# Kernel tuning notes

Hardware: AMD Instinct MI355X
Metric: run time of the kernel (lower is better)

Reference implementation:

```python
import jax, jax.numpy as jnp
import numpy as np
from functools import partial

N, C, D, H, W = 2, 64, 8, 96, 96
G, K, PAD = 2, 3, 1
P = K ** 3
CG = C // G
AXIS_SCALE = jnp.array([0.5, 1.0, 1.0], dtype=jnp.float32)  # applied to (dx, dy, dz)
OFFSET_SCALE = 1.0  # converged warmup scale
EPS = 1e-5


def setup_inputs() -> dict:
    key = jax.random.key(0)
    ks = jax.random.split(key, 13)
    s = 0.05
    return {
        "x": jax.random.normal(ks[0], (N, C, D, H, W), jnp.float32),
        "w_pre": jax.random.normal(ks[1], (C, C), jnp.float32) * s,
        "w_in": jax.random.normal(ks[2], (C, C), jnp.float32) * s,
        "b_in": jnp.zeros((C,), jnp.float32),
        "w_dw": jax.random.normal(ks[3], (C, 1, K, K, K), jnp.float32) * s,
        "w_off": jax.random.normal(ks[4], (C, G * P * 3), jnp.float32) * s,
        "b_off": jnp.zeros((G * P * 3,), jnp.float32),
        "w_mask": jax.random.normal(ks[5], (C, G * P), jnp.float32) * s,
        "b_mask": jnp.zeros((G * P,), jnp.float32),
        "w_out": jax.random.normal(ks[6], (C, C), jnp.float32) * s,
        "b_out": jnp.zeros((C,), jnp.float32),
        "w_post": jax.random.normal(ks[7], (C, C), jnp.float32) * s,
        "gate": jnp.zeros((), jnp.float32),
    }


def _instance_norm(x):  # x: [N, C, D, H, W], normalize over spatial dims per (n, c)
    mean = jnp.mean(x, axis=(2, 3, 4), keepdims=True)
    var = jnp.var(x, axis=(2, 3, 4), keepdims=True)
    return (x - mean) * jax.lax.rsqrt(var + EPS)


def _dcn_core(x_proj, offset, mask):
    # x_proj: [N, D, H, W, C]; offset: [N, D, H, W, G, P, 3] (dx, dy, dz); mask: [N, D, H, W, G, P]
    Dp, Hp, Wp = D + 2 * PAD, H + 2 * PAD, W + 2 * PAD
    x_pad = jnp.pad(x_proj, ((0, 0), (PAD, PAD), (PAD, PAD), (PAD, PAD), (0, 0)))
    x_pad = x_pad.reshape(N, Dp, Hp, Wp, G, CG)

    n_idx = jnp.arange(N).reshape(N, 1, 1, 1, 1)
    g_idx = jnp.arange(G).reshape(1, 1, 1, 1, G)
    zg = jnp.arange(D, dtype=jnp.float32).reshape(1, D, 1, 1, 1)
    yg = jnp.arange(H, dtype=jnp.float32).reshape(1, 1, H, 1, 1)
    xg = jnp.arange(W, dtype=jnp.float32).reshape(1, 1, 1, W, 1)

    def trilinear(zs, ys, xs):  # each [N, D, H, W, G] float coords in padded frame
        z0 = jnp.floor(zs); y0 = jnp.floor(ys); x0 = jnp.floor(xs)
        fz = zs - z0; fy = ys - y0; fx = xs - x0
        z0i = z0.astype(jnp.int32); y0i = y0.astype(jnp.int32); x0i = x0.astype(jnp.int32)
        res = None
        for dz in (0, 1):
            wz = fz if dz else 1.0 - fz
            zi = z0i + dz
            for dy in (0, 1):
                wy = fy if dy else 1.0 - fy
                yi = y0i + dy
                for dx in (0, 1):
                    wx = fx if dx else 1.0 - fx
                    xi = x0i + dx
                    valid = ((zi >= 0) & (zi < Dp) & (yi >= 0) & (yi < Hp)
                             & (xi >= 0) & (xi < Wp)).astype(zs.dtype)
                    g = x_pad[n_idx, jnp.clip(zi, 0, Dp - 1), jnp.clip(yi, 0, Hp - 1),
                              jnp.clip(xi, 0, Wp - 1), g_idx]  # [N,D,H,W,G,CG]
                    term = g * (wz * wy * wx * valid)[..., None]
                    res = term if res is None else res + term
        return res

    # kernel grid points (z-major), base position in padded frame is out_idx + k_idx
    kk = jnp.arange(K, dtype=jnp.float32)
    kz, ky, kx = jnp.meshgrid(kk, kk, kk, indexing="ij")
    kpts = jnp.stack([kz.ravel(), ky.ravel(), kx.ravel()], axis=-1)  # [P, 3]

    off = offset * (AXIS_SCALE * OFFSET_SCALE)  # scale (dx, dy, dz)
    off_p = jnp.moveaxis(off, 5, 0)    # [P, N, D, H, W, G, 3]
    mask_p = jnp.moveaxis(mask, 5, 0)  # [P, N, D, H, W, G]

    def body(acc, inp):
        o, m, kp = inp
        zs = zg + kp[0] + o[..., 2]
        ys = yg + kp[1] + o[..., 1]
        xs = xg + kp[2] + o[..., 0]
        samp = trilinear(zs, ys, xs)  # [N,D,H,W,G,CG]
        return acc + m[..., None] * samp, None

    acc0 = jnp.zeros((N, D, H, W, G, CG), x_proj.dtype)
    acc, _ = jax.lax.scan(body, acc0, (off_p, mask_p, kpts))
    return acc.reshape(N, D, H, W, C)


def _forward(x, w_pre, w_in, b_in, w_dw, w_off, b_off, w_mask, b_mask, w_out, b_out, w_post, gate):
    pre = jnp.einsum("ncdhw,oc->nodhw", x, w_pre)  # 1x1x1 conv, no bias
    x_cl = jnp.transpose(pre, (0, 2, 3, 4, 1))     # [N,D,H,W,C]
    x_proj = x_cl @ w_in + b_in
    # depthwise 3x3x3 conv + InstanceNorm + GELU for the offset/mask branch
    dw = jax.lax.conv_general_dilated(
        pre, w_dw, window_strides=(1, 1, 1), padding=((PAD, PAD),) * 3,
        feature_group_count=C, dimension_numbers=("NCDHW", "OIDHW", "NCDHW"))
    dw = jax.nn.gelu(_instance_norm(dw))
    feat = jnp.transpose(dw, (0, 2, 3, 4, 1))      # [N,D,H,W,C]
    offset = (feat @ w_off + b_off).reshape(N, D, H, W, G, P, 3)
    mask = jax.nn.softmax((feat @ w_mask + b_mask).reshape(N, D, H, W, G, P), axis=-1)
    core = _dcn_core(x_proj, offset, mask)         # [N,D,H,W,C]
    out = core @ w_out + b_out
    y = jnp.transpose(out, (0, 4, 1, 2, 3))        # back to NCDHW
    y = jnp.einsum("ncdhw,oc->nodhw", y, w_post)   # post 1x1x1 conv
    return x + jax.nn.sigmoid(gate) * y


def reference(x, w_pre, w_in, b_in, w_dw, w_off, b_off, w_mask, b_mask, w_out, b_out, w_post, gate):
    return _forward(x, w_pre, w_in, b_in, w_dw, w_off, b_off, w_mask, b_mask, w_out, b_out, w_post, gate)
```

## Files before the change

### kernel.cpp

```cpp
#include <hip/hip_runtime.h>
#include <math.h>

#define N_ 2
#define C_ 64
#define D_ 8
#define H_ 96
#define W_ 96
#define S_ (D_*H_*W_)
#define HW_ (H_*W_)
#define ZP_ 12
#define YP_ 100
#define XP_ 100
#define NSTR_ (ZP_*YP_*XP_*64)
#define ZS_ (YP_*XP_*64)
#define YS_ (XP_*64)

__device__ __forceinline__ float gelu_fast(float x) {
    float a = 0.7978845608028654f * (x + 0.044715f*x*x*x);
    float E = __expf(2.f*a);
    return x - x * __builtin_amdgcn_rcpf(E + 1.f);
}

__device__ __forceinline__ unsigned short f2bf(float f) {
    unsigned u = __float_as_uint(f);
    unsigned r = (u + 0x7fffu + ((u >> 16) & 1u)) >> 16;
    return (unsigned short)r;
}

__device__ __forceinline__ unsigned pkhi(float a, float b) {
    return __builtin_amdgcn_perm(__float_as_uint(a), __float_as_uint(b), 0x07060302u);
}

__global__ __launch_bounds__(64) void k_prep(const float* __restrict__ w_out,
        const float* __restrict__ b_out, const float* __restrict__ w_post,
        const float* __restrict__ w_off, const float* __restrict__ b_off,
        const float* __restrict__ w_mask, const float* __restrict__ b_mask,
        float* __restrict__ W2, float* __restrict__ B2,
        float4* __restrict__ woffT4, float4* __restrict__ b4f) {
    int b = blockIdx.x;
    int t = threadIdx.x;
    float acc = 0.f;
    for (int c = 0; c < 64; ++c)
        acc = fmaf(w_out[b*64+c], w_post[t*64+c], acc);
    W2[b*64 + t] = acc;
    if (b == 0) {
        float a2 = 0.f;
        for (int c = 0; c < 64; ++c)
            a2 = fmaf(w_post[t*64+c], b_out[c], a2);
        B2[t] = a2;
    }
    if (t < 54) {
        int c = b, u = t;
        woffT4[c*64 + u] = make_float4(w_off[c*162 + u*3] * 0.5f,
                                       w_off[c*162 + u*3 + 1],
                                       w_off[c*162 + u*3 + 2],
                                       w_mask[c*54 + u]);
        if (b == 1)
            b4f[u] = make_float4(b_off[u*3] * 0.5f, b_off[u*3+1], b_off[u*3+2],
                                 b_mask[u]);
    }
}

__global__ __launch_bounds__(256) void k_pre_proj(const float* __restrict__ x,
        const float* __restrict__ w_pre, const float* __restrict__ w_in,
        const float* __restrict__ b_in, float* __restrict__ pre,
        unsigned short* __restrict__ xprojP) {
    __shared__ float lx[64][65];
    __shared__ float lwa[64][65];
    __shared__ float lwb[64][65];
    int b = blockIdx.x;
    int n = b / 1152;
    int s0 = (b % 1152) * 64;
    int tid = threadIdx.x;
    for (int idx = tid; idx < 1024; idx += 256) {
        int r = idx >> 4, q4 = (idx & 15) * 4;
        float4 vx = *(const float4*)&x[((size_t)(n*C_ + r))*S_ + s0 + q4];
        lx[r][q4] = vx.x; lx[r][q4+1] = vx.y; lx[r][q4+2] = vx.z; lx[r][q4+3] = vx.w;
        float4 va = *(const float4*)&w_pre[r*64 + q4];
        lwa[r][q4] = va.x; lwa[r][q4+1] = va.y; lwa[r][q4+2] = va.z; lwa[r][q4+3] = va.w;
        float4 vb = *(const float4*)&w_in[r*64 + q4];
        lwb[r][q4] = vb.x; lwb[r][q4+1] = vb.y; lwb[r][q4+2] = vb.z; lwb[r][q4+3] = vb.w;
    }
    __syncthreads();
    int o0 = (tid & 15) * 4;
    int v0 = (tid >> 4) * 4;
    float acc[4][4] = {};
    #pragma unroll 8
    for (int c = 0; c < 64; ++c) {
        float xv[4], wv[4];
        #pragma unroll
        for (int j = 0; j < 4; ++j) { xv[j] = lx[c][v0+j]; wv[j] = lwa[o0+j][c]; }
        #pragma unroll
        for (int vj = 0; vj < 4; ++vj)
            #pragma unroll
            for (int oj = 0; oj < 4; ++oj)
                acc[vj][oj] = fmaf(xv[vj], wv[oj], acc[vj][oj]);
    }
    #pragma unroll
    for (int vj = 0; vj < 4; ++vj) {
        float4 r = make_float4(acc[vj][0], acc[vj][1], acc[vj][2], acc[vj][3]);
        *(float4*)&pre[((size_t)(n*S_ + s0 + v0 + vj))*64 + o0] = r;
    }
    __syncthreads();
    #pragma unroll
    for (int vj = 0; vj < 4; ++vj)
        #pragma unroll
        for (int oj = 0; oj < 4; ++oj)
            lx[v0+vj][o0+oj] = acc[vj][oj];
    __syncthreads();
    float acc2[4][4];
    #pragma unroll
    for (int oj = 0; oj < 4; ++oj) {
        float bo = b_in[o0+oj];
        #pragma unroll
        for (int vj = 0; vj < 4; ++vj) acc2[vj][oj] = bo;
    }
    #pragma unroll 8
    for (int c = 0; c < 64; ++c) {
        float fv[4], wv[4];
        #pragma unroll
        for (int j = 0; j < 4; ++j) { fv[j] = lx[v0+j][c]; wv[j] = lwb[c][o0+j]; }
        #pragma unroll
        for (int vj = 0; vj < 4; ++vj)
            #pragma unroll
            for (int oj = 0; oj < 4; ++oj)
                acc2[vj][oj] = fmaf(fv[vj], wv[oj], acc2[vj][oj]);
    }
    #pragma unroll
    for (int vj = 0; vj < 4; ++vj) {
        int vox = s0 + v0 + vj;
        int z = vox / HW_;
        int rem = vox - z*HW_;
        int y = rem / W_;
        int xq = rem - y*W_;
        size_t pw = (size_t)n*NSTR_ + (size_t)(z+2)*ZS_ + (y+2)*YS_ + (xq+2)*64 + o0;
        ushort4 pk;
        pk.x = f2bf(acc2[vj][0]); pk.y = f2bf(acc2[vj][1]);
        pk.z = f2bf(acc2[vj][2]); pk.w = f2bf(acc2[vj][3]);
        *(ushort4*)&xprojP[pw] = pk;
    }
}

__global__ __launch_bounds__(256) void k_dw_stats(const float* __restrict__ pre,
        const float* __restrict__ w_dw, float* __restrict__ dw,
        float* __restrict__ psum, float* __restrict__ pss) {
    __shared__ float4 lwd[27][16];
    __shared__ float4 lsum[16][16];
    __shared__ float4 lssum[16][16];
    int b = blockIdx.x;
    int y = b % H_;
    int z = (b / H_) % D_;
    int n = b / (D_*H_);
    int tid = threadIdx.x;
    if (tid < 27*16) {
        int k = tid >> 4, c4 = tid & 15;
        lwd[k][c4] = make_float4(w_dw[(c4*4+0)*27 + k], w_dw[(c4*4+1)*27 + k],
                                 w_dw[(c4*4+2)*27 + k], w_dw[(c4*4+3)*27 + k]);
    }
    __syncthreads();
    int c4 = tid & 15, xg = tid >> 4;
    const float* preN = pre + (size_t)n*S_*64;
    float4 s4 = make_float4(0,0,0,0), ss4 = make_float4(0,0,0,0);
    for (int xx = 0; xx < 6; ++xx) {
        int xi = xg + xx*16;
        float4 acc = make_float4(0,0,0,0);
        #pragma unroll
        for (int dz = 0; dz < 3; ++dz) {
            int zz = z + dz - 1;
            if (zz < 0 || zz >= D_) continue;
            #pragma unroll
            for (int dy = 0; dy < 3; ++dy) {
                int yy = y + dy - 1;
                if (yy < 0 || yy >= H_) continue;
                int rowb = (zz*HW_ + yy*W_)*64 + c4*4;
                #pragma unroll
                for (int dx = 0; dx < 3; ++dx) {
                    int xn = xi + dx - 1;
                    if ((unsigned)xn < (unsigned)W_) {
                        float4 v = *(const float4*)&preN[rowb + (xn<<6)];
                        float4 w = lwd[dz*9+dy*3+dx][c4];
                        acc.x = fmaf(v.x, w.x, acc.x);
                        acc.y = fmaf(v.y, w.y, acc.y);
                        acc.z = fmaf(v.z, w.z, acc.z);
                        acc.w = fmaf(v.w, w.w, acc.w);
                    }
                }
            }
        }
        *(float4*)&dw[((size_t)n*S_ + z*HW_ + y*W_ + xi)*64 + c4*4] = acc;
        s4.x += acc.x; s4.y += acc.y; s4.z += acc.z; s4.w += acc.w;
        ss4.x = fmaf(acc.x, acc.x, ss4.x); ss4.y = fmaf(acc.y, acc.y, ss4.y);
        ss4.z = fmaf(acc.z, acc.z, ss4.z); ss4.w = fmaf(acc.w, acc.w, ss4.w);
    }
    lsum[xg][c4] = s4; lssum[xg][c4] = ss4;
    __syncthreads();
    if (tid < 64) {
        float s = 0.f, ss = 0.f;
        #pragma unroll
        for (int k = 0; k < 16; ++k) {
            s  += ((const float*)&lsum [k][tid>>2])[tid&3];
            ss += ((const float*)&lssum[k][tid>>2])[tid&3];
        }
        psum[tid*1536 + b] = s;
        pss [tid*1536 + b] = ss;
    }
}

__global__ void k_stats2(const float* __restrict__ psum, const float* __restrict__ pss,
                         float* __restrict__ stats) {
    int u = blockIdx.x;
    int n = u >> 6, c = u & 63;
    int l = threadIdx.x;
    float s = 0.f, ss = 0.f;
    #pragma unroll
    for (int k = 0; k < 12; ++k) {
        int row = n*768 + k*64 + l;
        s  += psum[c*1536 + row];
        ss += pss [c*1536 + row];
    }
    #pragma unroll
    for (int o2 = 32; o2 >= 1; o2 >>= 1) {
        s  += __shfl_xor(s, o2);
        ss += __shfl_xor(ss, o2);
    }
    if (l == 0) {
        float inv = 1.f / (float)S_;
        float mean = s * inv;
        float var = ss * inv - mean*mean;
        stats[n*128 + c] = mean;
        stats[n*128 + 64 + c] = rsqrtf(var + 1e-5f);
    }
}

__global__ __launch_bounds__(256) void k_dcn(const unsigned short* __restrict__ xprojP,
        const float* __restrict__ dw, const float* __restrict__ stats,
        const float4* __restrict__ woffT4, const float4* __restrict__ b4f,
        unsigned short* __restrict__ coreB) {
    __shared__ union {
        float featT[64][36];
        int   cwl[64][27];
    } uS;
    __shared__ float4 offs4[64][29];
    int tid = threadIdx.x;
    int orig = blockIdx.x;
    int bid = (orig & 7) * 576 + (orig >> 3);
    int x8 = bid % 12;
    int t1 = bid / 12;
    int y4 = t1 % 24;
    int t2 = t1 / 24;
    int z  = t2 & 7;
    int n  = t2 >> 3;
    int yb = y4*4, xb = x8*8;
    size_t voxBase = (size_t)n*S_ + (size_t)z*HW_ + yb*W_ + xb;

    {
        int c4 = (tid & 15) * 4;
        int vp = tid >> 4;
        #pragma unroll
        for (int j = 0; j < 2; ++j) {
            int vloc = vp*2 + j;
            size_t vox = voxBase + (vloc>>3)*W_ + (vloc & 7);
            float4 v = *(const float4*)&dw[vox*64 + c4];
            float vals[4] = {v.x, v.y, v.z, v.w};
            #pragma unroll
            for (int jj = 0; jj < 4; ++jj) {
                int c = c4 + jj;
                float t = (vals[jj] - stats[n*128+c]) * stats[n*128+64+c];
                uS.featT[c][vloc] = gelu_fast(t);
            }
        }
    }
    __syncthreads();

    if (tid < 216) {
        int q = tid / 54;
        int u = tid - q*54;
        int g = u / 27, p = u - g*27;
        float4 bb = b4f[u];
        float4 aa[8];
        #pragma unroll
        for (int j = 0; j < 8; ++j) aa[j] = bb;
        for (int c = 0; c < 64; ++c) {
            float4 w = woffT4[c*64 + u];
            float4 f0 = *(const float4*)&uS.featT[c][q*8];
            float4 f1 = *(const float4*)&uS.featT[c][q*8 + 4];
            float ff[8] = {f0.x, f0.y, f0.z, f0.w, f1.x, f1.y, f1.z, f1.w};
            #pragma unroll
            for (int j = 0; j < 8; ++j) {
                aa[j].x = fmaf(ff[j], w.x, aa[j].x);
                aa[j].y = fmaf(ff[j], w.y, aa[j].y);
                aa[j].z = fmaf(ff[j], w.z, aa[j].z);
                aa[j].w = fmaf(ff[j], w.w, aa[j].w);
            }
        }
        #pragma unroll
        for (int j = 0; j < 8; ++j)
            offs4[(q*8+j)*2 + g][p] = aa[j];
    }
    __syncthreads();

    if (tid < 64) {
        float mx = -1e30f;
        #pragma unroll
        for (int p = 0; p < 27; ++p) mx = fmaxf(mx, offs4[tid][p].w);
        float e[27]; float ssum = 0.f;
        #pragma unroll
        for (int p = 0; p < 27; ++p) { e[p] = __expf(offs4[tid][p].w - mx); ssum += e[p]; }
        float inv = __builtin_amdgcn_rcpf(ssum);
        #pragma unroll
        for (int p = 0; p < 27; ++p) offs4[tid][p].w = e[p]*inv;
    }
    __syncthreads();

    {
        int zm1 = z - 1;
        #pragma unroll
        for (int k = 0; k < 7; ++k) {
            int idx = tid + k*256;
            if (idx < 1728) {
                int pair = idx / 27;
                int p = idx - pair*27;
                float4 tp = offs4[pair][p];
                int vloc = pair >> 1, g = pair & 1;
                int yy = vloc >> 3, xx = vloc & 7;
                float zf = (float)(zm1 + p/9) + tp.z;
                float yf = (float)(yb + yy - 1 + (p/3)%3) + tp.y;
                float xf = (float)(xb + xx - 1 + p%3) + tp.x;
                zf = fminf(fmaxf(zf, -1.5f), (float)D_ + 0.5f);
                yf = fminf(fmaxf(yf, -1.5f), (float)H_ + 0.5f);
                xf = fminf(fmaxf(xf, -1.5f), (float)W_ + 0.5f);
                float z0f = floorf(zf), y0f = floorf(yf), x0f = floorf(xf);
                float fz = zf - z0f, fy = yf - y0f, fx = xf - x0f;
                int zi = (int)z0f, yi = (int)y0f, xi = (int)x0f;
                float wz1 = fz * tp.w, wz0 = tp.w - wz1;
                float wy1 = fy, wy0 = 1.f - fy;
                float wx1 = fx, wx0 = 1.f - fx;
                float w00 = wz0*wy0, w01 = wz0*wy1, w10 = wz1*wy0, w11 = wz1*wy1;
                unsigned u0 = pkhi(w00*wx1, w00*wx0);
                unsigned u1 = pkhi(w01*wx1, w01*wx0);
                unsigned u2 = pkhi(w10*wx1, w10*wx0);
                unsigned u3 = pkhi(w11*wx1, w11*wx0);
                int cw = zi*ZS_ + yi*YS_ + (xi<<6) + (2*ZS_ + 2*YS_ + 128) + g*32;
                *(uint4*)&offs4[pair][p] = make_uint4(u0,u1,u2,u3);
                uS.cwl[pair][p] = cw;
            }
        }
    }
    __syncthreads();

    int pair = tid >> 2;
    int vloc = pair >> 1, g = pair & 1;
    int yy = vloc >> 3, xx = vloc & 7;
    int ch4 = (tid & 3) * 8;
    const unsigned short* __restrict__ base = xprojP + (size_t)n*NSTR_ + ch4;
    float a0=0.f,a1=0.f,a2=0.f,a3=0.f,a4=0.f,a5=0.f,a6=0.f,a7=0.f;
    #pragma unroll
    for (int p = 0; p < 27; ++p) {
        uint4 dsc = *(const uint4*)&offs4[pair][p];
        int cw = uS.cwl[pair][p];
        const unsigned short* p00 = base + cw;
        const unsigned short* p01 = p00 + YS_;
        const unsigned short* p10 = p00 + ZS_;
        const unsigned short* p11 = p10 + YS_;
        uint4 q000 = *(const uint4*)p00;
        uint4 q001 = *(const uint4*)(p00 + 64);
        uint4 q010 = *(const uint4*)p01;
        uint4 q011 = *(const uint4*)(p01 + 64);
        uint4 q100 = *(const uint4*)p10;
        uint4 q101 = *(const uint4*)(p10 + 64);
        uint4 q110 = *(const uint4*)p11;
        uint4 q111 = *(const uint4*)(p11 + 64);
        float c000 = __uint_as_float(dsc.x << 16), c001 = __uint_as_float(dsc.x);
        float c010 = __uint_as_float(dsc.y << 16), c011 = __uint_as_float(dsc.y);
        float c100 = __uint_as_float(dsc.z << 16), c101 = __uint_as_float(dsc.z);
        float c110 = __uint_as_float(dsc.w << 16), c111 = __uint_as_float(dsc.w);
        #define ACC8(Q, WGT) { \
            float wq = (WGT); \
            a0 = fmaf(wq, __uint_as_float((Q).x << 16), a0); \
            a1 = fmaf(wq, __uint_as_float((Q).x), a1); \
            a2 = fmaf(wq, __uint_as_float((Q).y << 16), a2); \
            a3 = fmaf(wq, __uint_as_float((Q).y), a3); \
            a4 = fmaf(wq, __uint_as_float((Q).z << 16), a4); \
            a5 = fmaf(wq, __uint_as_float((Q).z), a5); \
            a6 = fmaf(wq, __uint_as_float((Q).w << 16), a6); \
            a7 = fmaf(wq, __uint_as_float((Q).w), a7); \
        }
        ACC8(q000, c000); ACC8(q001, c001); ACC8(q010, c010); ACC8(q011, c011);
        ACC8(q100, c100); ACC8(q101, c101); ACC8(q110, c110); ACC8(q111, c111);
        #undef ACC8
    }
    size_t voxOut = voxBase + yy*W_ + xx;
    unsigned r01 = pkhi(a1, a0);
    unsigned r23 = pkhi(a3, a2);
    unsigned r45 = pkhi(a5, a4);
    unsigned r67 = pkhi(a7, a6);
    *(uint4*)&coreB[voxOut*64 + g*32 + ch4] = make_uint4(r01, r23, r45, r67);
}

__global__ __launch_bounds__(256) void k_final(const unsigned short* __restrict__ coreB,
        const float* __restrict__ W2, const float* __restrict__ B2,
        const float* __restrict__ x, const float* __restrict__ gate,
        float* __restrict__ out) {
    __shared__ float lc[64][65];
    __shared__ float lw[64][65];
    int b = blockIdx.x;
    int n = b / 1152;
    int s0 = (b % 1152) * 64;
    int tid = threadIdx.x;
    for (int idx = tid; idx < 512; idx += 256) {
        int r = idx >> 3, q8 = (idx & 7) * 8;
        uint4 q = *(const uint4*)&coreB[((size_t)(n*S_ + s0 + r))*64 + q8];
        lc[r][q8+0] = __uint_as_float(q.x << 16);
        lc[r][q8+1] = __uint_as_float(q.x & 0xffff0000u);
        lc[r][q8+2] = __uint_as_float(q.y << 16);
        lc[r][q8+3] = __uint_as_float(q.y & 0xffff0000u);
        lc[r][q8+4] = __uint_as_float(q.z << 16);
        lc[r][q8+5] = __uint_as_float(q.z & 0xffff0000u);
        lc[r][q8+6] = __uint_as_float(q.w << 16);
        lc[r][q8+7] = __uint_as_float(q.w & 0xffff0000u);
    }
    for (int idx = tid; idx < 1024; idx += 256) {
        int r = idx >> 4, q4 = (idx & 15) * 4;
        float4 vw = *(const float4*)&W2[r*64 + q4];
        lw[r][q4] = vw.x; lw[r][q4+1] = vw.y; lw[r][q4+2] = vw.z; lw[r][q4+3] = vw.w;
    }
    __syncthreads();
    float sg = 1.f / (1.f + expf(-gate[0]));
    int o0 = (tid & 15) * 4;
    int v0 = (tid >> 4) * 4;
    float acc[4][4];
    #pragma unroll
    for (int oj = 0; oj < 4; ++oj) {
        float bo = B2[o0+oj];
        #pragma unroll
        for (int vj = 0; vj < 4; ++vj) acc[vj][oj] = bo;
    }
    #pragma unroll 8
    for (int c = 0; c < 64; ++c) {
        float fv[4], wv[4];
        #pragma unroll
        for (int j = 0; j < 4; ++j) { fv[j] = lc[v0+j][c]; wv[j] = lw[c][o0+j]; }
        #pragma unroll
        for (int vj = 0; vj < 4; ++vj)
            #pragma unroll
            for (int oj = 0; oj < 4; ++oj)
                acc[vj][oj] = fmaf(fv[vj], wv[oj], acc[vj][oj]);
    }
    #pragma unroll
    for (int oj = 0; oj < 4; ++oj) {
        size_t gi = ((size_t)(n*64 + o0 + oj))*S_ + s0 + v0;
        float4 xv = *(const float4*)&x[gi];
        float4 r;
        r.x = fmaf(sg, acc[0][oj], xv.x);
        r.y = fmaf(sg, acc[1][oj], xv.y);
        r.z = fmaf(sg, acc[2][oj], xv.z);
        r.w = fmaf(sg, acc[3][oj], xv.w);
        *(float4*)&out[gi] = r;
    }
}

extern "C" void kernel_launch(void* const* d_in, const int* in_sizes, int n_in,
                              void* d_out, int out_size, void* d_ws, size_t ws_size,
                              hipStream_t stream) {
    const float* x      = (const float*)d_in[0];
    const float* w_pre  = (const float*)d_in[1];
    const float* w_in   = (const float*)d_in[2];
    const float* b_in   = (const float*)d_in[3];
    const float* w_dw   = (const float*)d_in[4];
    const float* w_off  = (const float*)d_in[5];
    const float* b_off  = (const float*)d_in[6];
    const float* w_mask = (const float*)d_in[7];
    const float* b_mask = (const float*)d_in[8];
    const float* w_out  = (const float*)d_in[9];
    const float* b_out  = (const float*)d_in[10];
    const float* w_post = (const float*)d_in[11];
    const float* gate   = (const float*)d_in[12];
    float* out = (float*)d_out;

    float* ws      = (float*)d_ws;
    unsigned short* xprojP = (unsigned short*)ws;
    float* pre     = ws + (size_t)7680000;
    unsigned short* coreB = (unsigned short*)(pre + (size_t)9437184);
    float* psum    = (float*)(coreB + (size_t)9437184);
    float* pss     = psum + 98304;
    float* stats   = pss + 98304;
    float* W2      = stats + 256;
    float* B2      = W2 + 4096;
    float4* woffT4 = (float4*)(B2 + 128);
    float4* b4f    = woffT4 + 4096;
    float* dwb     = out;

    hipMemsetAsync(xprojP, 0, (size_t)15360000*sizeof(unsigned short), stream);
    hipLaunchKernelGGL(k_prep,     dim3(64),   dim3(64),  0, stream,
                       w_out, b_out, w_post, w_off, b_off, w_mask, b_mask,
                       W2, B2, woffT4, b4f);
    hipLaunchKernelGGL(k_pre_proj, dim3(2304), dim3(256), 0, stream,
                       x, w_pre, w_in, b_in, pre, xprojP);
    hipLaunchKernelGGL(k_dw_stats, dim3(1536), dim3(256), 0, stream,
                       pre, w_dw, dwb, psum, pss);
    hipLaunchKernelGGL(k_stats2,   dim3(128),  dim3(64),  0, stream, psum, pss, stats);
    hipLaunchKernelGGL(k_dcn,      dim3(4608), dim3(256), 0, stream,
                       xprojP, dwb, stats, woffT4, b4f, coreB);
    hipLaunchKernelGGL(k_final,    dim3(2304), dim3(256), 0, stream,
                       coreB, W2, B2, x, gate, out);
}
```

Measured before the change: 329.4 us.

## Compute offset/mask projection in k_dcn with bf16 MFMA instead of scalar FMA

The per-block offset/mask projection (32 voxels x 64 channels x 216 outputs) now runs on bf16 MFMA 16x16x32 instructions instead of scalar fp32 FMAs. The GELU features are packed to bf16 in an XOR-swizzled shared tile, and the prep kernel writes a bf16 weight matrix padded to 224 rows. This removes a large VALU cost and leaves all four waves busy instead of 216 threads. In exchange, offsets and mask logits are computed at bf16 input precision, which can move sampling positions slightly.

```diff
diff --git a/kernel.cpp b/kernel.cpp
--- a/kernel.cpp
+++ b/kernel.cpp
@@ -15,6 +15,9 @@
 #define ZS_ (YP_*XP_*64)
 #define YS_ (XP_*64)
 
+typedef __attribute__((ext_vector_type(8))) short short8;
+typedef __attribute__((ext_vector_type(4))) float f32x4;
+
 __device__ __forceinline__ float gelu_fast(float x) {
     float a = 0.7978845608028654f * (x + 0.044715f*x*x*x);
     float E = __expf(2.f*a);
@@ -36,7 +39,7 @@
         const float* __restrict__ w_off, const float* __restrict__ b_off,
         const float* __restrict__ w_mask, const float* __restrict__ b_mask,
         float* __restrict__ W2, float* __restrict__ B2,
-        float4* __restrict__ woffT4, float4* __restrict__ b4f) {
+        unsigned short* __restrict__ wBg, float4* __restrict__ b4f) {
     int b = blockIdx.x;
     int t = threadIdx.x;
     float acc = 0.f;
@@ -49,16 +52,23 @@
             a2 = fmaf(w_post[t*64+c], b_out[c], a2);
         B2[t] = a2;
     }
-    if (t < 54) {
-        int c = b, u = t;
-        woffT4[c*64 + u] = make_float4(w_off[c*162 + u*3] * 0.5f,
-                                       w_off[c*162 + u*3 + 1],
-                                       w_off[c*162 + u*3 + 2],
-                                       w_mask[c*54 + u]);
-        if (b == 1)
-            b4f[u] = make_float4(b_off[u*3] * 0.5f, b_off[u*3+1], b_off[u*3+2],
-                                 b_mask[u]);
-    }
+    {
+        int c = b;
+        for (int m = t; m < 224; m += 64) {
+            float v = 0.f;
+            if (m < 216) {
+                int u = m >> 2, comp = m & 3;
+                if (comp == 3) v = w_mask[c*54 + u];
+                else {
+                    v = w_off[c*162 + u*3 + comp];
+                    if (comp == 0) v *= 0.5f;
+                }
+            }
+            wBg[m*64 + c] = f2bf(v);
+        }
+    }
+    if (b == 1 && t < 54)
+        b4f[t] = make_float4(b_off[t*3]*0.5f, b_off[t*3+1], b_off[t*3+2], b_mask[t]);
 }
 
 __global__ __launch_bounds__(256) void k_pre_proj(const float* __restrict__ x,
@@ -234,11 +244,11 @@
 
 __global__ __launch_bounds__(256) void k_dcn(const unsigned short* __restrict__ xprojP,
         const float* __restrict__ dw, const float* __restrict__ stats,
-        const float4* __restrict__ woffT4, const float4* __restrict__ b4f,
+        const unsigned short* __restrict__ wBg, const float4* __restrict__ b4f,
         unsigned short* __restrict__ coreB) {
     __shared__ union {
-        float featT[64][36];
-        int   cwl[64][27];
+        unsigned short featB[32][64];
+        int cwl[64][27];
     } uS;
     __shared__ float4 offs4[64][29];
     int tid = threadIdx.x;
@@ -262,40 +272,47 @@
             size_t vox = voxBase + (vloc>>3)*W_ + (vloc & 7);
             float4 v = *(const float4*)&dw[vox*64 + c4];
             float vals[4] = {v.x, v.y, v.z, v.w};
+            ushort4 pk;
+            unsigned short* pp = (unsigned short*)&pk;
             #pragma unroll
             for (int jj = 0; jj < 4; ++jj) {
                 int c = c4 + jj;
                 float t = (vals[jj] - stats[n*128+c]) * stats[n*128+64+c];
-                uS.featT[c][vloc] = gelu_fast(t);
+                pp[jj] = f2bf(gelu_fast(t));
             }
-        }
-    }
-    __syncthreads();
-
-    if (tid < 216) {
-        int q = tid / 54;
-        int u = tid - q*54;
-        int g = u / 27, p = u - g*27;
-        float4 bb = b4f[u];
-        float4 aa[8];
-        #pragma unroll
-        for (int j = 0; j < 8; ++j) aa[j] = bb;
-        for (int c = 0; c < 64; ++c) {
-            float4 w = woffT4[c*64 + u];
-            float4 f0 = *(const float4*)&uS.featT[c][q*8];
-            float4 f1 = *(const float4*)&uS.featT[c][q*8 + 4];
-            float ff[8] = {f0.x, f0.y, f0.z, f0.w, f1.x, f1.y, f1.z, f1.w};
+            int off = ((((c4 >> 3) ^ (vloc & 7)) << 3) | (c4 & 7));
+            *(ushort4*)&uS.featB[vloc][off] = pk;
+        }
+    }
+    __syncthreads();
+
+    {
+        int w = tid >> 6;
+        int l = tid & 63;
+        int lr = l & 15;
+        int lq = l >> 4;
+        for (int i = 0; i < 7; ++i) {
+            int t7 = w*7 + i;
+            int mt = t7 >> 1, nt = t7 & 1;
+            int vox = nt*16 + lr;
+            f32x4 acc = {0.f, 0.f, 0.f, 0.f};
             #pragma unroll
-            for (int j = 0; j < 8; ++j) {
-                aa[j].x = fmaf(ff[j], w.x, aa[j].x);
-                aa[j].y = fmaf(ff[j], w.y, aa[j].y);
-                aa[j].z = fmaf(ff[j], w.z, aa[j].z);
-                aa[j].w = fmaf(ff[j], w.w, aa[j].w);
+            for (int h = 0; h < 2; ++h) {
+                int k0 = h*32 + lq*8;
+                short8 af = *(const short8*)&wBg[(mt*16 + lr)*64 + k0];
+                int blk = (((k0 >> 3) ^ (vox & 7)) << 3);
+                short8 bf = *(const short8*)&uS.featB[vox][blk];
+                acc = __builtin_amdgcn_mfma_f32_16x16x32_bf16(af, bf, acc, 0, 0, 0);
             }
-        }
-        #pragma unroll
-        for (int j = 0; j < 8; ++j)
-            offs4[(q*8+j)*2 + g][p] = aa[j];
+            int u = mt*4 + lq;
+            if (u < 54) {
+                float4 bb = b4f[u];
+                int g = (u >= 27) ? 1 : 0;
+                int p = u - g*27;
+                offs4[vox*2 + g][p] = make_float4(acc[0] + bb.x, acc[1] + bb.y,
+                                                  acc[2] + bb.z, acc[3] + bb.w);
+            }
+        }
     }
     __syncthreads();
 
@@ -486,21 +503,21 @@
     float* stats   = pss + 98304;
     float* W2      = stats + 256;
     float* B2      = W2 + 4096;
-    float4* woffT4 = (float4*)(B2 + 128);
-    float4* b4f    = woffT4 + 4096;
+    unsigned short* wBg = (unsigned short*)(B2 + 128);
+    float4* b4f    = (float4*)(B2 + 128 + 7168);
     float* dwb     = out;
 
     hipMemsetAsync(xprojP, 0, (size_t)15360000*sizeof(unsigned short), stream);
     hipLaunchKernelGGL(k_prep,     dim3(64),   dim3(64),  0, stream,
                        w_out, b_out, w_post, w_off, b_off, w_mask, b_mask,
-                       W2, B2, woffT4, b4f);
+                       W2, B2, wBg, b4f);
     hipLaunchKernelGGL(k_pre_proj, dim3(2304), dim3(256), 0, stream,
                        x, w_pre, w_in, b_in, pre, xprojP);
     hipLaunchKernelGGL(k_dw_stats, dim3(1536), dim3(256), 0, stream,
                        pre, w_dw, dwb, psum, pss);
     hipLaunchKernelGGL(k_stats2,   dim3(128),  dim3(64),  0, stream, psum, pss, stats);
     hipLaunchKernelGGL(k_dcn,      dim3(4608), dim3(256), 0, stream,
-                       xprojP, dwb, stats, woffT4, b4f, coreB);
+                       xprojP, dwb, stats, wBg, b4f, coreB);
     hipLaunchKernelGGL(k_final,    dim3(2304), dim3(256), 0, stream,
                        coreB, W2, B2, x, gate, out);
 }
```

After: 324.5 us. No clear change (-1.5%).
